# Performance work log

Measured on AMD Instinct MI355X. Metric: run time of the kernel, lower is better.

Reference implementation:

```python
import jax, jax.numpy as jnp
import numpy as np

B, C_IN, H, T = 64, 256, 512, 1024
TMAX = 1024
EPS = 1e-5  # torch LayerNorm default


def setup_inputs() -> dict:
    key = jax.random.key(0)
    ks = jax.random.split(key, 8)
    std = 1.0 / np.sqrt(H)
    u = lambda k, shape: jax.random.uniform(k, shape, jnp.float32, -std, std)
    xs = jax.random.normal(ks[0], (B, C_IN, T), jnp.float32)
    # Linear weights (torch layout [out, in]); LayerNorm gamma=0.1, beta=0,
    # except h2h beta[H:2H] = log(Uniform(1, Tmax-1))  (chrono-style init).
    def ln_h2h_bias(k):
        b = jnp.zeros((3 * H,), jnp.float32)
        z = jnp.log(jax.random.uniform(k, (H,), jnp.float32, 1.0, TMAX - 1.0))
        return b.at[H:2 * H].set(z)
    gamma = jnp.full((3 * H,), 0.1, jnp.float32)
    beta0 = jnp.zeros((3 * H,), jnp.float32)
    return {
        "xs": xs,
        "Wx0": u(ks[1], (3 * H, C_IN)), "Wh0": u(ks[2], (3 * H, H)),
        "gx0": gamma, "bx0": beta0, "gh0": gamma, "bh0": ln_h2h_bias(ks[3]),
        "Wx1": u(ks[4], (3 * H, H)), "Wh1": u(ks[5], (3 * H, H)),
        "gx1": gamma, "bx1": beta0, "gh1": gamma, "bh1": ln_h2h_bias(ks[6]),
    }


def _ln(z, g, b):
    m = jnp.mean(z, axis=-1, keepdims=True)
    v = jnp.mean((z - m) ** 2, axis=-1, keepdims=True)
    return (z - m) * jax.lax.rsqrt(v + EPS) * g + b


def _cell(x, h, Wx, Wh, gx, bx, gh, bh):
    gate_x = _ln(x @ Wx.T, gx, bx)          # [B, 3H]
    gate_h = _ln(h @ Wh.T, gh, bh)          # [B, 3H]
    i_r, i_i, i_n = jnp.split(gate_x, 3, axis=-1)
    h_r, h_i, h_n = jnp.split(gate_h, 3, axis=-1)
    r = jax.nn.sigmoid(i_r + h_r)
    ig = jax.nn.sigmoid(i_i + h_i)
    n = jnp.tanh(i_n + r * h_n)
    return n + ig * (h - n)


def reference(xs, Wx0, Wh0, gx0, bx0, gh0, bh0, Wx1, Wh1, gx1, bx1, gh1, bh1):
    p0 = (Wx0, Wh0, gx0, bx0, gh0, bh0)
    p1 = (Wx1, Wh1, gx1, bx1, gh1, bh1)
    xs_t = jnp.transpose(xs, (2, 0, 1))  # [T, B, C_IN]
    h_init = (jnp.zeros((B, H), xs.dtype), jnp.zeros((B, H), xs.dtype))

    def step(carry, x):
        h0, h1 = carry
        h0 = _cell(x, h0, *p0)
        h1 = _cell(h0, h1, *p1)
        return (h0, h1), h1

    _, ys = jax.lax.scan(step, h_init, xs_t)  # [T, B, H]
    return jnp.transpose(ys, (1, 2, 0))       # [B, H, T]
```

## Files before the change

kernel.cpp:

```cpp
#include <hip/hip_runtime.h>
#include <hip/hip_bf16.h>
#include <cstdint>
#include <cstddef>


#define NBATCH 64
#define HDIM   512
#define THREE_H 1536
#define CINDIM 256
#define T_STEPS 1024
#define EPSLN 1e-5f
#define NBLK 64

typedef __bf16 bf8v __attribute__((ext_vector_type(8)));
typedef float f4 __attribute__((ext_vector_type(4)));
typedef float f2 __attribute__((ext_vector_type(2)));
typedef unsigned int u32x4 __attribute__((ext_vector_type(4)));

static constexpr size_t OFF_BAR    = 0;
static constexpr size_t OFF_ST0P   = 8192;
static constexpr size_t OFF_ST1P   = 24576;
static constexpr size_t OFF_ST2P   = 40960;
static constexpr size_t OFF_H0BF   = 57344;
static constexpr size_t OFF_H1BF   = 122880;
static constexpr size_t OFF_STATSX = 188416;
static constexpr size_t OFF_WH0HI  = 712704;
static constexpr size_t OFF_WH0LO  = OFF_WH0HI + 1572864;
static constexpr size_t OFF_WX1HI  = OFF_WH0LO + 1572864;
static constexpr size_t OFF_WX1LO  = OFF_WX1HI + 1572864;
static constexpr size_t OFF_WH1HI  = OFF_WX1LO + 1572864;
static constexpr size_t OFF_WH1LO  = OFF_WH1HI + 1572864;
static constexpr size_t OFF_WX0HI  = OFF_WH1LO + 1572864;
static constexpr size_t OFF_WX0LO  = OFF_WX0HI + 786432;
static constexpr size_t OFF_XST    = OFF_WX0LO + 786432;
static constexpr size_t OFF_GX0    = OFF_XST + 33554432;

__device__ __forceinline__ f4 mf(bf8v a, bf8v b, f4 c){
  return __builtin_amdgcn_mfma_f32_16x16x32_bf16(a, b, c, 0, 0, 0);
}
__device__ __forceinline__ float sigf(float x){ return 1.0f/(1.0f + __expf(-x)); }
__device__ __forceinline__ float tanhfast(float x){ return 1.0f - 2.0f/(__expf(2.0f*x) + 1.0f); }

__device__ __forceinline__ bf8v ld16_cross(const void* p){
  u32x4 t;
  asm volatile("global_load_dwordx4 %0, %1, off sc0 sc1" : "=v"(t) : "v"(p));
  return __builtin_bit_cast(bf8v, t);
}
__device__ __forceinline__ f4 ld16f_cross(const float* p){
  f4 v;
  asm volatile("global_load_dwordx4 %0, %1, off sc0 sc1" : "=v"(v) : "v"(p));
  return v;
}
__device__ __forceinline__ void st2_cross(__hip_bfloat16* p, unsigned int u){
  asm volatile("global_store_short %0, %1, off sc0 sc1" :: "v"(p), "v"(u));
}
__device__ __forceinline__ void st8f_cross(float* p, f2 v){
  asm volatile("global_store_dwordx2 %0, %1, off sc0 sc1" :: "v"(p), "v"(v));
}
__device__ __forceinline__ void vm_drain(){
  asm volatile("s_waitcnt vmcnt(0)" ::: "memory");
  __builtin_amdgcn_sched_barrier(0);
}

__device__ __forceinline__ void gbar(unsigned int* flags, unsigned int target){
  asm volatile("s_waitcnt vmcnt(0) lgkmcnt(0)" ::: "memory");
  __syncthreads();
  if (threadIdx.x == 0){
    unsigned int* myf = flags + (size_t)blockIdx.x * 32;
    asm volatile("global_store_dword %0, %1, off sc0 sc1" :: "v"(myf), "v"(target) : "memory");
  }
  const int lane = threadIdx.x & 63;
  const unsigned int* pf = flags + (size_t)lane * 32;
  for (;;){
    unsigned int v;
    asm volatile("global_load_dword %0, %1, off sc0 sc1\n\ts_waitcnt vmcnt(0)"
                 : "=v"(v) : "v"(pf) : "memory");
    if (__all((int)(v >= target))) break;
    __builtin_amdgcn_s_sleep(1);
  }
}

__global__ void k_zero(unsigned int* p, int nwords){
  for (int i = blockIdx.x*blockDim.x + threadIdx.x; i < nwords; i += gridDim.x*blockDim.x)
    p[i] = 0u;
}

__global__ void k_conv(const float* __restrict__ src, __hip_bfloat16* __restrict__ hi,
                       __hip_bfloat16* __restrict__ lo, int n){
  for (int i = blockIdx.x*blockDim.x + threadIdx.x; i < n; i += gridDim.x*blockDim.x){
    float w = src[i];
    __hip_bfloat16 h = __float2bfloat16(w);
    hi[i] = h;
    lo[i] = __float2bfloat16(w - __bfloat162float(h));
  }
}

__global__ void k_tr(const float* __restrict__ xs, __hip_bfloat16* __restrict__ xsT){
  const int total = NBATCH * CINDIM * (T_STEPS/4);
  for (int idx = blockIdx.x*blockDim.x + threadIdx.x; idx < total; idx += gridDim.x*blockDim.x){
    int b  = idx >> 16;
    int c  = (idx >> 8) & 255;
    int t4 = idx & 255;
    const float4 v = *(const float4*)(xs + ((size_t)b*CINDIM + c)*T_STEPS + t4*4);
    float vv[4] = {v.x, v.y, v.z, v.w};
    #pragma unroll
    for (int i = 0; i < 4; ++i)
      xsT[(size_t)(4*t4 + i)*(NBATCH*CINDIM) + b*CINDIM + c] = __float2bfloat16(vv[i]);
  }
}

__global__ __launch_bounds__(256,1) void k_xgemm(unsigned char* __restrict__ ws){
  const int tid = threadIdx.x;
  const int bx = blockIdx.x;
  const int t = bx >> 4, s = bx & 15;
  const int lane = tid & 63, w = tid >> 6, l15 = lane & 15, lg = lane >> 4;

  const __hip_bfloat16* X  = (const __hip_bfloat16*)(ws + OFF_XST) + (size_t)t*(NBATCH*CINDIM);
  const __hip_bfloat16* WH = (const __hip_bfloat16*)(ws + OFF_WX0HI);
  const __hip_bfloat16* WL = (const __hip_bfloat16*)(ws + OFF_WX0LO);
  float* statsX = (float*)(ws + OFF_STATSX);
  __hip_bfloat16* GX0 = (__hip_bfloat16*)(ws + OFF_GX0) + (size_t)t*(NBATCH*THREE_H);

  __shared__ __hip_bfloat16 SB[2][2][96][72];

  f4 acc[6];
  #pragma unroll
  for (int i = 0; i < 6; ++i) acc[i] = f4{0.f,0.f,0.f,0.f};

  bf8v A0[8];
  #pragma unroll
  for (int kk = 0; kk < 8; ++kk)
    A0[kk] = *(const bf8v*)(X + (16*w + l15)*CINDIM + kk*32 + 8*lg);

  bf8v pre[6];
  #pragma unroll
  for (int rep = 0; rep < 6; ++rep){
    int idx = tid + rep*256; int half = idx >= 768 ? 1 : 0; int i2 = idx - half*768;
    int rr = i2 >> 3, ko = (i2 & 7)*8;
    int j = 32*s + (rr & 31) + 512*(rr >> 5);
    const __hip_bfloat16* sp = (half ? WL : WH) + (size_t)j*CINDIM;
    pre[rep] = *(const bf8v*)(sp + ko);
  }
  #pragma unroll
  for (int chk = 0; chk < 4; ++chk){
    #pragma unroll
    for (int rep = 0; rep < 6; ++rep){
      int idx = tid + rep*256; int half = idx >= 768 ? 1 : 0; int i2 = idx - half*768;
      int rr = i2 >> 3, ko = (i2 & 7)*8;
      *(bf8v*)&SB[chk & 1][half][rr][ko] = pre[rep];
    }
    __syncthreads();
    if (chk < 3){
      #pragma unroll
      for (int rep = 0; rep < 6; ++rep){
        int idx = tid + rep*256; int half = idx >= 768 ? 1 : 0; int i2 = idx - half*768;
        int rr = i2 >> 3, ko = (i2 & 7)*8;
        int j = 32*s + (rr & 31) + 512*(rr >> 5);
        const __hip_bfloat16* sp = (half ? WL : WH) + (size_t)j*CINDIM;
        pre[rep] = *(const bf8v*)(sp + (chk+1)*64 + ko);
      }
    }
    #pragma unroll
    for (int sub = 0; sub < 2; ++sub){
      int kk = 2*chk + sub; int ko = 32*sub + 8*lg;
      bf8v a = A0[kk];
      #pragma unroll
      for (int nf = 0; nf < 6; ++nf){
        bf8v bh = *(const bf8v*)&SB[chk & 1][0][16*nf + l15][ko];
        bf8v bl = *(const bf8v*)&SB[chk & 1][1][16*nf + l15][ko];
        acc[nf] = mf(a, bh, acc[nf]);
        acc[nf] = mf(a, bl, acc[nf]);
      }
    }
  }

  #pragma unroll
  for (int r = 0; r < 4; ++r){
    int row = 16*w + 4*lg + r;
    float sm = 0.f, sq = 0.f;
    #pragma unroll
    for (int nf = 0; nf < 6; ++nf){
      float v = acc[nf][r];
      sm += v; sq += v*v;
      int tc = 16*nf + l15;
      int j = 32*s + (tc & 31) + 512*(tc >> 5);
      GX0[(size_t)row*THREE_H + j] = __float2bfloat16(v);
    }
    #pragma unroll
    for (int m = 1; m < 16; m <<= 1){ sm += __shfl_xor(sm, m); sq += __shfl_xor(sq, m); }
    if (l15 == 0){
      atomicAdd(&statsX[((size_t)t*64 + row)*2 + 0], sm);
      atomicAdd(&statsX[((size_t)t*64 + row)*2 + 1], sq);
    }
  }
}

__global__ void k_statsx(float* __restrict__ sx){
  int i = blockIdx.x*blockDim.x + threadIdx.x;
  if (i < T_STEPS*NBATCH){
    float s = sx[2*i], q = sx[2*i+1];
    float m = s * (1.0f/1536.0f);
    float v = fmaxf(q * (1.0f/1536.0f) - m*m, 0.0f);
    sx[2*i] = m;
    sx[2*i+1] = rsqrtf(v + EPSLN);
  }
}


__device__ __forceinline__ void runA(
    int s, unsigned char* ws, f4* red, f2* BC0,
    const float* gxg, const float* gxb, const float* ghg, const float* ghb)
{
  const int tid = threadIdx.x, lane = tid & 63, w = tid >> 6;
  const int l15 = lane & 15, lg = (lane >> 4) & 3;

  unsigned int* flags = (unsigned int*)(ws + OFF_BAR);
  float* st0P = (float*)(ws + OFF_ST0P);
  __hip_bfloat16* h0bf = (__hip_bfloat16*)(ws + OFF_H0BF);
  const float* statsX = (const float*)(ws + OFF_STATSX);
  const __hip_bfloat16* GX0 = (const __hip_bfloat16*)(ws + OFF_GX0);

  bf8v BW[3][4][2];
  {
    const __hip_bfloat16* hi = (const __hip_bfloat16*)(ws + OFF_WH0HI);
    const __hip_bfloat16* lo = (const __hip_bfloat16*)(ws + OFF_WH0LO);
    #pragma unroll
    for (int g = 0; g < 3; ++g){
      const size_t j = (size_t)(16*s + l15 + 512*g);
      #pragma unroll
      for (int kt = 0; kt < 4; ++kt){
        const size_t ko = (size_t)((4*w + kt)*32 + 8*lg);
        BW[g][kt][0] = *(const bf8v*)(hi + j*HDIM + ko);
        BW[g][kt][1] = *(const bf8v*)(lo + j*HDIM + ko);
      }
    }
  }
  float PXg[3], PXb[3], PHg[3], PHb[3];
  #pragma unroll
  for (int g = 0; g < 3; ++g){
    int j = 16*s + l15 + 512*g;
    PXg[g] = gxg[j]; PXb[g] = gxb[j]; PHg[g] = ghg[j]; PHb[g] = ghb[j];
  }

  float hp[4] = {0.f,0.f,0.f,0.f};
  unsigned int bc = 0;

  for (int tau = 0; tau <= T_STEPS; ++tau){
    const bool act = (tau < T_STEPS);
    f4 zx[3];
    float gxraw[3][4], mxv[4], rsxv[4];

    if (act){
      bf8v AR[4][4];
      #pragma unroll
      for (int rt = 0; rt < 4; ++rt)
        #pragma unroll
        for (int kt = 0; kt < 4; ++kt)
          AR[rt][kt] = ld16_cross(h0bf + (size_t)(16*rt + l15)*HDIM + (4*w + kt)*32 + 8*lg);
      vm_drain();

      f4 AC[3][4];
      #pragma unroll
      for (int g = 0; g < 3; ++g)
        #pragma unroll
        for (int rt = 0; rt < 4; ++rt) AC[g][rt] = f4{0.f,0.f,0.f,0.f};
      #pragma unroll
      for (int kt = 0; kt < 4; ++kt)
        #pragma unroll
        for (int g = 0; g < 3; ++g)
          #pragma unroll
          for (int rt = 0; rt < 4; ++rt){
            AC[g][rt] = mf(AR[rt][kt], BW[g][kt][0], AC[g][rt]);
            AC[g][rt] = mf(AR[rt][kt], BW[g][kt][1], AC[g][rt]);
          }

      #pragma unroll
      for (int r = 0; r < 4; ++r){
        int row = 16*w + 4*lg + r;
        mxv[r]  = statsX[((size_t)tau*64 + row)*2 + 0];
        rsxv[r] = statsX[((size_t)tau*64 + row)*2 + 1];
        #pragma unroll
        for (int g = 0; g < 3; ++g)
          gxraw[g][r] = __bfloat162float(
            GX0[(size_t)tau*(NBATCH*THREE_H) + (size_t)row*THREE_H + (16*s + l15 + 512*g)]);
      }

      #pragma unroll
      for (int g = 0; g < 3; ++g)
        #pragma unroll
        for (int rt = 0; rt < 4; ++rt)
          red[((w*3 + g)*4 + rt)*64 + lane] = AC[g][rt];
      __syncthreads();
      #pragma unroll
      for (int g = 0; g < 3; ++g){
        f4 a = red[((0*3 + g)*4 + w)*64 + lane];
        a += red[((1*3 + g)*4 + w)*64 + lane];
        a += red[((2*3 + g)*4 + w)*64 + lane];
        a += red[((3*3 + g)*4 + w)*64 + lane];
        zx[g] = a;
      }

      #pragma unroll
      for (int r = 0; r < 4; ++r){
        float s1 = zx[0][r] + zx[1][r] + zx[2][r];
        float q1 = zx[0][r]*zx[0][r] + zx[1][r]*zx[1][r] + zx[2][r]*zx[2][r];
        #pragma unroll
        for (int m = 1; m < 16; m <<= 1){ s1 += __shfl_xor(s1, m); q1 += __shfl_xor(q1, m); }
        if (l15 == 0){
          int row = 16*w + 4*lg + r;
          st8f_cross(st0P + ((size_t)row*32 + s)*2, f2{s1, q1});
        }
      }
    }

    gbar(flags, ++bc);

    if (act){
      {
        int row = tid >> 2, q = tid & 3;
        const float* bp = st0P + (size_t)row*64 + q*16;
        f4 v0 = ld16f_cross(bp),   v1 = ld16f_cross(bp+4);
        f4 v2 = ld16f_cross(bp+8), v3 = ld16f_cross(bp+12);
        vm_drain();
        float sm = v0[0]+v0[2]+v1[0]+v1[2]+v2[0]+v2[2]+v3[0]+v3[2];
        float sq = v0[1]+v0[3]+v1[1]+v1[3]+v2[1]+v2[3]+v3[1]+v3[3];
        sm += __shfl_xor(sm,1); sq += __shfl_xor(sq,1);
        sm += __shfl_xor(sm,2); sq += __shfl_xor(sq,2);
        if (q == 0){
          float m = sm*(1.0f/1536.0f);
          float vv = fmaxf(sq*(1.0f/1536.0f) - m*m, 0.0f);
          BC0[row] = f2{m, rsqrtf(vv + EPSLN)};
        }
      }
      __syncthreads();
      #pragma unroll
      for (int r = 0; r < 4; ++r){
        int row = 16*w + 4*lg + r;
        f2 mr = BC0[row];
        float m = mr[0], rs = mr[1];
        float ghr = (zx[0][r]-m)*rs*PHg[0] + PHb[0];
        float ghi = (zx[1][r]-m)*rs*PHg[1] + PHb[1];
        float ghn = (zx[2][r]-m)*rs*PHg[2] + PHb[2];
        float gxr = (gxraw[0][r] - mxv[r])*rsxv[r]*PXg[0] + PXb[0];
        float gxi = (gxraw[1][r] - mxv[r])*rsxv[r]*PXg[1] + PXb[1];
        float gxn = (gxraw[2][r] - mxv[r])*rsxv[r]*PXg[2] + PXb[2];
        float rg = sigf(gxr + ghr);
        float ig = sigf(gxi + ghi);
        float nn = tanhfast(gxn + rg*ghn);
        float hn = nn + ig*(hp[r] - nn);
        hp[r] = hn;
        __hip_bfloat16 hb = __float2bfloat16(hn);
        st2_cross(h0bf + (size_t)row*HDIM + 16*s + l15,
                  (unsigned int)*reinterpret_cast<unsigned short*>(&hb));
      }
    }

    gbar(flags, ++bc);
  }
}

__device__ __forceinline__ void runB(
    int s, unsigned char* ws, f4* red, f2* BC1, f2* BC2,
    const float* gxg, const float* gxb, const float* ghg, const float* ghb,
    float* out)
{
  const int tid = threadIdx.x, lane = tid & 63, w = tid >> 6;
  const int l15 = lane & 15, lg = (lane >> 4) & 3;

  unsigned int* flags = (unsigned int*)(ws + OFF_BAR);
  float* st1P = (float*)(ws + OFF_ST1P);
  float* st2P = (float*)(ws + OFF_ST2P);
  __hip_bfloat16* h0bf = (__hip_bfloat16*)(ws + OFF_H0BF);
  __hip_bfloat16* h1bf = (__hip_bfloat16*)(ws + OFF_H1BF);

  bf8v BW[6][4][2];
  {
    const __hip_bfloat16* hix = (const __hip_bfloat16*)(ws + OFF_WX1HI);
    const __hip_bfloat16* lox = (const __hip_bfloat16*)(ws + OFF_WX1LO);
    const __hip_bfloat16* hih = (const __hip_bfloat16*)(ws + OFF_WH1HI);
    const __hip_bfloat16* loh = (const __hip_bfloat16*)(ws + OFF_WH1LO);
    #pragma unroll
    for (int g = 0; g < 3; ++g){
      const size_t j = (size_t)(16*s + l15 + 512*g);
      #pragma unroll
      for (int kt = 0; kt < 4; ++kt){
        const size_t ko = (size_t)((4*w + kt)*32 + 8*lg);
        BW[g][kt][0]   = *(const bf8v*)(hix + j*HDIM + ko);
        BW[g][kt][1]   = *(const bf8v*)(lox + j*HDIM + ko);
        BW[3+g][kt][0] = *(const bf8v*)(hih + j*HDIM + ko);
        BW[3+g][kt][1] = *(const bf8v*)(loh + j*HDIM + ko);
      }
    }
  }
  float PXg[3], PXb[3], PHg[3], PHb[3];
  #pragma unroll
  for (int g = 0; g < 3; ++g){
    int j = 16*s + l15 + 512*g;
    PXg[g] = gxg[j]; PXb[g] = gxb[j]; PHg[g] = ghg[j]; PHb[g] = ghb[j];
  }

  float hp[4] = {0.f,0.f,0.f,0.f};
  unsigned int bc = 0;

  for (int tau = 0; tau <= T_STEPS; ++tau){
    const bool act = (tau >= 1);
    f4 zx[3], zh[3];

    if (act){
      bf8v AR[4][4];
      #pragma unroll
      for (int rt = 0; rt < 4; ++rt)
        #pragma unroll
        for (int kt = 0; kt < 4; ++kt)
          AR[rt][kt] = ld16_cross(h0bf + (size_t)(16*rt + l15)*HDIM + (4*w + kt)*32 + 8*lg);
      vm_drain();

      f4 AC[3][4];
      #pragma unroll
      for (int g = 0; g < 3; ++g)
        #pragma unroll
        for (int rt = 0; rt < 4; ++rt) AC[g][rt] = f4{0.f,0.f,0.f,0.f};
      #pragma unroll
      for (int kt = 0; kt < 4; ++kt)
        #pragma unroll
        for (int g = 0; g < 3; ++g)
          #pragma unroll
          for (int rt = 0; rt < 4; ++rt){
            AC[g][rt] = mf(AR[rt][kt], BW[g][kt][0], AC[g][rt]);
            AC[g][rt] = mf(AR[rt][kt], BW[g][kt][1], AC[g][rt]);
          }
      #pragma unroll
      for (int g = 0; g < 3; ++g)
        #pragma unroll
        for (int rt = 0; rt < 4; ++rt)
          red[((w*3 + g)*4 + rt)*64 + lane] = AC[g][rt];

      #pragma unroll
      for (int rt = 0; rt < 4; ++rt)
        #pragma unroll
        for (int kt = 0; kt < 4; ++kt)
          AR[rt][kt] = ld16_cross(h1bf + (size_t)(16*rt + l15)*HDIM + (4*w + kt)*32 + 8*lg);

      __syncthreads();
      #pragma unroll
      for (int g = 0; g < 3; ++g){
        f4 a = red[((0*3 + g)*4 + w)*64 + lane];
        a += red[((1*3 + g)*4 + w)*64 + lane];
        a += red[((2*3 + g)*4 + w)*64 + lane];
        a += red[((3*3 + g)*4 + w)*64 + lane];
        zx[g] = a;
      }
      __syncthreads();

      vm_drain();
      #pragma unroll
      for (int g = 0; g < 3; ++g)
        #pragma unroll
        for (int rt = 0; rt < 4; ++rt) AC[g][rt] = f4{0.f,0.f,0.f,0.f};
      #pragma unroll
      for (int kt = 0; kt < 4; ++kt)
        #pragma unroll
        for (int g = 0; g < 3; ++g)
          #pragma unroll
          for (int rt = 0; rt < 4; ++rt){
            AC[g][rt] = mf(AR[rt][kt], BW[3+g][kt][0], AC[g][rt]);
            AC[g][rt] = mf(AR[rt][kt], BW[3+g][kt][1], AC[g][rt]);
          }
      #pragma unroll
      for (int g = 0; g < 3; ++g)
        #pragma unroll
        for (int rt = 0; rt < 4; ++rt)
          red[((w*3 + g)*4 + rt)*64 + lane] = AC[g][rt];
      __syncthreads();
      #pragma unroll
      for (int g = 0; g < 3; ++g){
        f4 a = red[((0*3 + g)*4 + w)*64 + lane];
        a += red[((1*3 + g)*4 + w)*64 + lane];
        a += red[((2*3 + g)*4 + w)*64 + lane];
        a += red[((3*3 + g)*4 + w)*64 + lane];
        zh[g] = a;
      }

      #pragma unroll
      for (int r = 0; r < 4; ++r){
        float s1 = zx[0][r] + zx[1][r] + zx[2][r];
        float q1 = zx[0][r]*zx[0][r] + zx[1][r]*zx[1][r] + zx[2][r]*zx[2][r];
        float s2 = zh[0][r] + zh[1][r] + zh[2][r];
        float q2 = zh[0][r]*zh[0][r] + zh[1][r]*zh[1][r] + zh[2][r]*zh[2][r];
        #pragma unroll
        for (int m = 1; m < 16; m <<= 1){
          s1 += __shfl_xor(s1, m); q1 += __shfl_xor(q1, m);
          s2 += __shfl_xor(s2, m); q2 += __shfl_xor(q2, m);
        }
        if (l15 == 0){
          int row = 16*w + 4*lg + r;
          st8f_cross(st1P + ((size_t)row*32 + s)*2, f2{s1, q1});
          st8f_cross(st2P + ((size_t)row*32 + s)*2, f2{s2, q2});
        }
      }
    }

    gbar(flags, ++bc);

    if (act){
      const int t1 = tau - 1;
      {
        int row = tid >> 2, q = tid & 3;
        const float* b1 = st1P + (size_t)row*64 + q*16;
        const float* b2 = st2P + (size_t)row*64 + q*16;
        f4 a0 = ld16f_cross(b1),   a1 = ld16f_cross(b1+4);
        f4 a2 = ld16f_cross(b1+8), a3 = ld16f_cross(b1+12);
        f4 c0 = ld16f_cross(b2),   c1 = ld16f_cross(b2+4);
        f4 c2 = ld16f_cross(b2+8), c3 = ld16f_cross(b2+12);
        vm_drain();
        float s1 = a0[0]+a0[2]+a1[0]+a1[2]+a2[0]+a2[2]+a3[0]+a3[2];
        float q1 = a0[1]+a0[3]+a1[1]+a1[3]+a2[1]+a2[3]+a3[1]+a3[3];
        float s2 = c0[0]+c0[2]+c1[0]+c1[2]+c2[0]+c2[2]+c3[0]+c3[2];
        float q2 = c0[1]+c0[3]+c1[1]+c1[3]+c2[1]+c2[3]+c3[1]+c3[3];
        s1 += __shfl_xor(s1,1); q1 += __shfl_xor(q1,1);
        s1 += __shfl_xor(s1,2); q1 += __shfl_xor(q1,2);
        s2 += __shfl_xor(s2,1); q2 += __shfl_xor(q2,1);
        s2 += __shfl_xor(s2,2); q2 += __shfl_xor(q2,2);
        if (q == 0){
          float m1 = s1*(1.0f/1536.0f);
          float v1 = fmaxf(q1*(1.0f/1536.0f) - m1*m1, 0.0f);
          BC1[row] = f2{m1, rsqrtf(v1 + EPSLN)};
          float m2 = s2*(1.0f/1536.0f);
          float v2 = fmaxf(q2*(1.0f/1536.0f) - m2*m2, 0.0f);
          BC2[row] = f2{m2, rsqrtf(v2 + EPSLN)};
        }
      }
      __syncthreads();
      #pragma unroll
      for (int r = 0; r < 4; ++r){
        int row = 16*w + 4*lg + r;
        f2 m1 = BC1[row], m2 = BC2[row];
        float gxr = (zx[0][r] - m1[0])*m1[1]*PXg[0] + PXb[0];
        float gxi = (zx[1][r] - m1[0])*m1[1]*PXg[1] + PXb[1];
        float gxn = (zx[2][r] - m1[0])*m1[1]*PXg[2] + PXb[2];
        float ghr = (zh[0][r] - m2[0])*m2[1]*PHg[0] + PHb[0];
        float ghi = (zh[1][r] - m2[0])*m2[1]*PHg[1] + PHb[1];
        float ghn = (zh[2][r] - m2[0])*m2[1]*PHg[2] + PHb[2];
        float rg = sigf(gxr + ghr);
        float ig = sigf(gxi + ghi);
        float nn = tanhfast(gxn + rg*ghn);
        float hn = nn + ig*(hp[r] - nn);
        hp[r] = hn;
        int j = 16*s + l15;
        __hip_bfloat16 hb = __float2bfloat16(hn);
        st2_cross(h1bf + (size_t)row*HDIM + j,
                  (unsigned int)*reinterpret_cast<unsigned short*>(&hb));
        out[(size_t)row*(HDIM*T_STEPS) + (size_t)j*T_STEPS + t1] = hn;
      }
    }

    gbar(flags, ++bc);
  }
}

__global__ __launch_bounds__(256,1) void k_rnn(
    const float* __restrict__ gx0g, const float* __restrict__ gx0b,
    const float* __restrict__ gh0g, const float* __restrict__ gh0b,
    const float* __restrict__ gx1g, const float* __restrict__ gx1b,
    const float* __restrict__ gh1g, const float* __restrict__ gh1b,
    unsigned char* __restrict__ ws, float* __restrict__ out)
{
  __shared__ f4 red[4*3*4*64];
  __shared__ f2 BCa[64];
  __shared__ f2 BCb[64];

  const int bi = blockIdx.x;
  if (bi < 32)
    runA(bi, ws, red, BCa, gx0g, gx0b, gh0g, gh0b);
  else
    runB(bi - 32, ws, red, BCa, BCb, gx1g, gx1b, gh1g, gh1b, out);
}

extern "C" void kernel_launch(void* const* d_in, const int* in_sizes, int n_in,
                              void* d_out, int out_size, void* d_ws, size_t ws_size,
                              hipStream_t stream) {
  const float* xs  = (const float*)d_in[0];
  const float* Wx0 = (const float*)d_in[1];
  const float* Wh0 = (const float*)d_in[2];
  const float* gx0g = (const float*)d_in[3];
  const float* gx0b = (const float*)d_in[4];
  const float* gh0g = (const float*)d_in[5];
  const float* gh0b = (const float*)d_in[6];
  const float* Wx1 = (const float*)d_in[7];
  const float* Wh1 = (const float*)d_in[8];
  const float* gx1g = (const float*)d_in[9];
  const float* gx1b = (const float*)d_in[10];
  const float* gh1g = (const float*)d_in[11];
  const float* gh1b = (const float*)d_in[12];

  unsigned char* ws = (unsigned char*)d_ws;
  float* out = (float*)d_out;
  (void)in_sizes; (void)n_in; (void)out_size; (void)ws_size;

  k_zero<<<256, 256, 0, stream>>>((unsigned int*)ws, (int)(OFF_WH0HI/4));

  k_conv<<<512, 256, 0, stream>>>(Wh0, (__hip_bfloat16*)(ws+OFF_WH0HI), (__hip_bfloat16*)(ws+OFF_WH0LO), THREE_H*HDIM);
  k_conv<<<512, 256, 0, stream>>>(Wx1, (__hip_bfloat16*)(ws+OFF_WX1HI), (__hip_bfloat16*)(ws+OFF_WX1LO), THREE_H*HDIM);
  k_conv<<<512, 256, 0, stream>>>(Wh1, (__hip_bfloat16*)(ws+OFF_WH1HI), (__hip_bfloat16*)(ws+OFF_WH1LO), THREE_H*HDIM);
  k_conv<<<512, 256, 0, stream>>>(Wx0, (__hip_bfloat16*)(ws+OFF_WX0HI), (__hip_bfloat16*)(ws+OFF_WX0LO), THREE_H*CINDIM);

  k_tr<<<4096, 256, 0, stream>>>(xs, (__hip_bfloat16*)(ws+OFF_XST));

  k_xgemm<<<16384, 256, 0, stream>>>(ws);
  k_statsx<<<256, 256, 0, stream>>>((float*)(ws+OFF_STATSX));

  k_rnn<<<NBLK, 256, 0, stream>>>(gx0g, gx0b, gh0g, gh0b, gx1g, gx1b, gh1g, gh1b, ws, out);
}
```

Before: 13.02 ms.

## Replace global barriers with per-group flags, epoch-tagged stats, and multi-buffered hidden states

Removes the two full-grid barriers per timestep and replaces them with point-to-point flag polling. Layer-0 blocks wait only on their own group and on layer 1 being at most three steps behind. Layer-1 blocks wait on the matching layer-0 step. LayerNorm partial stats now carry an epoch tag, so readers spin on the data itself instead of a barrier. h0 is ring-buffered four deep and h1 double-buffered, letting the two layers run decoupled and pipelined, at the cost of more workspace and spin-polling traffic.

```diff
diff --git a/kernel.cpp b/kernel.cpp
--- a/kernel.cpp
+++ b/kernel.cpp
@@ -11,6 +11,7 @@
 #define T_STEPS 1024
 #define EPSLN 1e-5f
 #define NBLK 64
+#define HSZ (NBATCH*HDIM)
 
 typedef __bf16 bf8v __attribute__((ext_vector_type(8)));
 typedef float f4 __attribute__((ext_vector_type(4)));
@@ -18,13 +19,13 @@
 typedef unsigned int u32x4 __attribute__((ext_vector_type(4)));
 
 static constexpr size_t OFF_BAR    = 0;
-static constexpr size_t OFF_ST0P   = 8192;
-static constexpr size_t OFF_ST1P   = 24576;
-static constexpr size_t OFF_ST2P   = 40960;
-static constexpr size_t OFF_H0BF   = 57344;
-static constexpr size_t OFF_H1BF   = 122880;
-static constexpr size_t OFF_STATSX = 188416;
-static constexpr size_t OFF_WH0HI  = 712704;
+static constexpr size_t OFF_STA    = 8192;
+static constexpr size_t OFF_STB1   = 40960;
+static constexpr size_t OFF_STB2   = 73728;
+static constexpr size_t OFF_H0BF   = 106496;
+static constexpr size_t OFF_H1BF   = 368640;
+static constexpr size_t OFF_STATSX = 499712;
+static constexpr size_t OFF_WH0HI  = 1024000;
 static constexpr size_t OFF_WH0LO  = OFF_WH0HI + 1572864;
 static constexpr size_t OFF_WX1HI  = OFF_WH0LO + 1572864;
 static constexpr size_t OFF_WX1LO  = OFF_WX1HI + 1572864;
@@ -54,30 +55,30 @@
 __device__ __forceinline__ void st2_cross(__hip_bfloat16* p, unsigned int u){
   asm volatile("global_store_short %0, %1, off sc0 sc1" :: "v"(p), "v"(u));
 }
-__device__ __forceinline__ void st8f_cross(float* p, f2 v){
-  asm volatile("global_store_dwordx2 %0, %1, off sc0 sc1" :: "v"(p), "v"(v));
+__device__ __forceinline__ void st16f_cross(float* p, f4 v){
+  asm volatile("global_store_dwordx4 %0, %1, off sc0 sc1" :: "v"(p), "v"(v));
 }
 __device__ __forceinline__ void vm_drain(){
   asm volatile("s_waitcnt vmcnt(0)" ::: "memory");
   __builtin_amdgcn_sched_barrier(0);
 }
 
-__device__ __forceinline__ void gbar(unsigned int* flags, unsigned int target){
-  asm volatile("s_waitcnt vmcnt(0) lgkmcnt(0)" ::: "memory");
-  __syncthreads();
-  if (threadIdx.x == 0){
-    unsigned int* myf = flags + (size_t)blockIdx.x * 32;
-    asm volatile("global_store_dword %0, %1, off sc0 sc1" :: "v"(myf), "v"(target) : "memory");
-  }
+__device__ __forceinline__ void dualpoll(const unsigned int* flags, unsigned tA, unsigned tB){
   const int lane = threadIdx.x & 63;
   const unsigned int* pf = flags + (size_t)lane * 32;
+  const unsigned tgt = (lane < 32) ? tA : tB;
   for (;;){
     unsigned int v;
     asm volatile("global_load_dword %0, %1, off sc0 sc1\n\ts_waitcnt vmcnt(0)"
                  : "=v"(v) : "v"(pf) : "memory");
-    if (__all((int)(v >= target))) break;
+    if (__all((int)(v >= tgt))) break;
     __builtin_amdgcn_s_sleep(1);
   }
+}
+
+__device__ __forceinline__ void pubflag(unsigned int* flags, int line, unsigned val){
+  unsigned int* p = flags + (size_t)line * 32;
+  asm volatile("global_store_dword %0, %1, off sc0 sc1" :: "v"(p), "v"(val) : "memory");
 }
 
 __global__ void k_zero(unsigned int* p, int nwords){
@@ -215,7 +216,7 @@
   const int l15 = lane & 15, lg = (lane >> 4) & 3;
 
   unsigned int* flags = (unsigned int*)(ws + OFF_BAR);
-  float* st0P = (float*)(ws + OFF_ST0P);
+  float* stA = (float*)(ws + OFF_STA);
   __hip_bfloat16* h0bf = (__hip_bfloat16*)(ws + OFF_H0BF);
   const float* statsX = (const float*)(ws + OFF_STATSX);
   const __hip_bfloat16* GX0 = (const __hip_bfloat16*)(ws + OFF_GX0);
@@ -243,119 +244,130 @@
   }
 
   float hp[4] = {0.f,0.f,0.f,0.f};
-  unsigned int bc = 0;
-
-  for (int tau = 0; tau <= T_STEPS; ++tau){
-    const bool act = (tau < T_STEPS);
-    f4 zx[3];
-    float gxraw[3][4], mxv[4], rsxv[4];
-
-    if (act){
-      bf8v AR[4][4];
-      #pragma unroll
-      for (int rt = 0; rt < 4; ++rt)
-        #pragma unroll
-        for (int kt = 0; kt < 4; ++kt)
-          AR[rt][kt] = ld16_cross(h0bf + (size_t)(16*rt + l15)*HDIM + (4*w + kt)*32 + 8*lg);
-      vm_drain();
-
-      f4 AC[3][4];
+
+  for (int t = 0; t < T_STEPS; ++t){
+    const float ef = (float)(t + 1);
+    const unsigned tB = (t >= 3) ? (unsigned)(t - 3) : 0u;
+
+    dualpoll(flags, (unsigned)t, tB);
+
+    const __hip_bfloat16* h0r = h0bf + (size_t)((t + 3) & 3) * HSZ;
+    __hip_bfloat16*       h0w = h0bf + (size_t)(t & 3) * HSZ;
+
+    bf8v AR[4][4];
+    #pragma unroll
+    for (int rt = 0; rt < 4; ++rt)
+      #pragma unroll
+      for (int kt = 0; kt < 4; ++kt)
+        AR[rt][kt] = ld16_cross(h0r + (size_t)(16*rt + l15)*HDIM + (4*w + kt)*32 + 8*lg);
+    vm_drain();
+
+    f4 AC[3][4];
+    #pragma unroll
+    for (int g = 0; g < 3; ++g)
+      #pragma unroll
+      for (int rt = 0; rt < 4; ++rt) AC[g][rt] = f4{0.f,0.f,0.f,0.f};
+    #pragma unroll
+    for (int kt = 0; kt < 4; ++kt)
       #pragma unroll
       for (int g = 0; g < 3; ++g)
         #pragma unroll
-        for (int rt = 0; rt < 4; ++rt) AC[g][rt] = f4{0.f,0.f,0.f,0.f};
-      #pragma unroll
-      for (int kt = 0; kt < 4; ++kt)
+        for (int rt = 0; rt < 4; ++rt){
+          AC[g][rt] = mf(AR[rt][kt], BW[g][kt][0], AC[g][rt]);
+          AC[g][rt] = mf(AR[rt][kt], BW[g][kt][1], AC[g][rt]);
+        }
+
+    float gxraw[3][4], mxv[4], rsxv[4];
+    #pragma unroll
+    for (int r = 0; r < 4; ++r){
+      int row = 16*w + 4*lg + r;
+      mxv[r]  = statsX[((size_t)t*64 + row)*2 + 0];
+      rsxv[r] = statsX[((size_t)t*64 + row)*2 + 1];
+      #pragma unroll
+      for (int g = 0; g < 3; ++g)
+        gxraw[g][r] = __bfloat162float(
+          GX0[(size_t)t*(NBATCH*THREE_H) + (size_t)row*THREE_H + (16*s + l15 + 512*g)]);
+    }
+
+    f4 zx[3];
+    #pragma unroll
+    for (int g = 0; g < 3; ++g)
+      #pragma unroll
+      for (int rt = 0; rt < 4; ++rt)
+        red[((w*3 + g)*4 + rt)*64 + lane] = AC[g][rt];
+    __syncthreads();
+    #pragma unroll
+    for (int g = 0; g < 3; ++g){
+      f4 a = red[((0*3 + g)*4 + w)*64 + lane];
+      a += red[((1*3 + g)*4 + w)*64 + lane];
+      a += red[((2*3 + g)*4 + w)*64 + lane];
+      a += red[((3*3 + g)*4 + w)*64 + lane];
+      zx[g] = a;
+    }
+
+    #pragma unroll
+    for (int r = 0; r < 4; ++r){
+      float s1 = zx[0][r] + zx[1][r] + zx[2][r];
+      float q1 = zx[0][r]*zx[0][r] + zx[1][r]*zx[1][r] + zx[2][r]*zx[2][r];
+      #pragma unroll
+      for (int m = 1; m < 16; m <<= 1){ s1 += __shfl_xor(s1, m); q1 += __shfl_xor(q1, m); }
+      if (l15 == 0){
+        int row = 16*w + 4*lg + r;
+        st16f_cross(stA + ((size_t)row*32 + s)*4, f4{s1, q1, ef, 0.f});
+      }
+    }
+
+    {
+      int row = tid >> 2, q = tid & 3;
+      const float* bp = stA + ((size_t)row*32 + q*8)*4;
+      f4 v[8];
+      for (;;){
         #pragma unroll
-        for (int g = 0; g < 3; ++g)
-          #pragma unroll
-          for (int rt = 0; rt < 4; ++rt){
-            AC[g][rt] = mf(AR[rt][kt], BW[g][kt][0], AC[g][rt]);
-            AC[g][rt] = mf(AR[rt][kt], BW[g][kt][1], AC[g][rt]);
-          }
-
-      #pragma unroll
-      for (int r = 0; r < 4; ++r){
-        int row = 16*w + 4*lg + r;
-        mxv[r]  = statsX[((size_t)tau*64 + row)*2 + 0];
-        rsxv[r] = statsX[((size_t)tau*64 + row)*2 + 1];
+        for (int i = 0; i < 8; ++i) v[i] = ld16f_cross(bp + i*4);
+        vm_drain();
+        bool ok = true;
         #pragma unroll
-        for (int g = 0; g < 3; ++g)
-          gxraw[g][r] = __bfloat162float(
-            GX0[(size_t)tau*(NBATCH*THREE_H) + (size_t)row*THREE_H + (16*s + l15 + 512*g)]);
-      }
-
-      #pragma unroll
-      for (int g = 0; g < 3; ++g)
-        #pragma unroll
-        for (int rt = 0; rt < 4; ++rt)
-          red[((w*3 + g)*4 + rt)*64 + lane] = AC[g][rt];
-      __syncthreads();
-      #pragma unroll
-      for (int g = 0; g < 3; ++g){
-        f4 a = red[((0*3 + g)*4 + w)*64 + lane];
-        a += red[((1*3 + g)*4 + w)*64 + lane];
-        a += red[((2*3 + g)*4 + w)*64 + lane];
-        a += red[((3*3 + g)*4 + w)*64 + lane];
-        zx[g] = a;
-      }
-
-      #pragma unroll
-      for (int r = 0; r < 4; ++r){
-        float s1 = zx[0][r] + zx[1][r] + zx[2][r];
-        float q1 = zx[0][r]*zx[0][r] + zx[1][r]*zx[1][r] + zx[2][r]*zx[2][r];
-        #pragma unroll
-        for (int m = 1; m < 16; m <<= 1){ s1 += __shfl_xor(s1, m); q1 += __shfl_xor(q1, m); }
-        if (l15 == 0){
-          int row = 16*w + 4*lg + r;
-          st8f_cross(st0P + ((size_t)row*32 + s)*2, f2{s1, q1});
-        }
-      }
-    }
-
-    gbar(flags, ++bc);
-
-    if (act){
-      {
-        int row = tid >> 2, q = tid & 3;
-        const float* bp = st0P + (size_t)row*64 + q*16;
-        f4 v0 = ld16f_cross(bp),   v1 = ld16f_cross(bp+4);
-        f4 v2 = ld16f_cross(bp+8), v3 = ld16f_cross(bp+12);
-        vm_drain();
-        float sm = v0[0]+v0[2]+v1[0]+v1[2]+v2[0]+v2[2]+v3[0]+v3[2];
-        float sq = v0[1]+v0[3]+v1[1]+v1[3]+v2[1]+v2[3]+v3[1]+v3[3];
-        sm += __shfl_xor(sm,1); sq += __shfl_xor(sq,1);
-        sm += __shfl_xor(sm,2); sq += __shfl_xor(sq,2);
-        if (q == 0){
-          float m = sm*(1.0f/1536.0f);
-          float vv = fmaxf(sq*(1.0f/1536.0f) - m*m, 0.0f);
-          BC0[row] = f2{m, rsqrtf(vv + EPSLN)};
-        }
-      }
-      __syncthreads();
-      #pragma unroll
-      for (int r = 0; r < 4; ++r){
-        int row = 16*w + 4*lg + r;
-        f2 mr = BC0[row];
-        float m = mr[0], rs = mr[1];
-        float ghr = (zx[0][r]-m)*rs*PHg[0] + PHb[0];
-        float ghi = (zx[1][r]-m)*rs*PHg[1] + PHb[1];
-        float ghn = (zx[2][r]-m)*rs*PHg[2] + PHb[2];
-        float gxr = (gxraw[0][r] - mxv[r])*rsxv[r]*PXg[0] + PXb[0];
-        float gxi = (gxraw[1][r] - mxv[r])*rsxv[r]*PXg[1] + PXb[1];
-        float gxn = (gxraw[2][r] - mxv[r])*rsxv[r]*PXg[2] + PXb[2];
-        float rg = sigf(gxr + ghr);
-        float ig = sigf(gxi + ghi);
-        float nn = tanhfast(gxn + rg*ghn);
-        float hn = nn + ig*(hp[r] - nn);
-        hp[r] = hn;
-        __hip_bfloat16 hb = __float2bfloat16(hn);
-        st2_cross(h0bf + (size_t)row*HDIM + 16*s + l15,
-                  (unsigned int)*reinterpret_cast<unsigned short*>(&hb));
-      }
-    }
-
-    gbar(flags, ++bc);
+        for (int i = 0; i < 8; ++i) ok = ok && (v[i][2] >= ef);
+        if (__all((int)ok)) break;
+        __builtin_amdgcn_s_sleep(1);
+      }
+      float sm = 0.f, sq = 0.f;
+      #pragma unroll
+      for (int i = 0; i < 8; ++i){ sm += v[i][0]; sq += v[i][1]; }
+      sm += __shfl_xor(sm,1); sq += __shfl_xor(sq,1);
+      sm += __shfl_xor(sm,2); sq += __shfl_xor(sq,2);
+      if (q == 0){
+        float m = sm*(1.0f/1536.0f);
+        float vv = fmaxf(sq*(1.0f/1536.0f) - m*m, 0.0f);
+        BC0[row] = f2{m, rsqrtf(vv + EPSLN)};
+      }
+    }
+    __syncthreads();
+
+    #pragma unroll
+    for (int r = 0; r < 4; ++r){
+      int row = 16*w + 4*lg + r;
+      f2 mr = BC0[row];
+      float m = mr[0], rs = mr[1];
+      float ghr = (zx[0][r]-m)*rs*PHg[0] + PHb[0];
+      float ghi = (zx[1][r]-m)*rs*PHg[1] + PHb[1];
+      float ghn = (zx[2][r]-m)*rs*PHg[2] + PHb[2];
+      float gxr = (gxraw[0][r] - mxv[r])*rsxv[r]*PXg[0] + PXb[0];
+      float gxi = (gxraw[1][r] - mxv[r])*rsxv[r]*PXg[1] + PXb[1];
+      float gxn = (gxraw[2][r] - mxv[r])*rsxv[r]*PXg[2] + PXb[2];
+      float rg = sigf(gxr + ghr);
+      float ig = sigf(gxi + ghi);
+      float nn = tanhfast(gxn + rg*ghn);
+      float hn = nn + ig*(hp[r] - nn);
+      hp[r] = hn;
+      __hip_bfloat16 hb = __float2bfloat16(hn);
+      st2_cross(h0w + (size_t)row*HDIM + 16*s + l15,
+                (unsigned int)*reinterpret_cast<unsigned short*>(&hb));
+    }
+
+    vm_drain();
+    __syncthreads();
+    if (tid == 0) pubflag(flags, s, (unsigned)(t + 1));
   }
 }
 
@@ -368,8 +380,8 @@
   const int l15 = lane & 15, lg = (lane >> 4) & 3;
 
   unsigned int* flags = (unsigned int*)(ws + OFF_BAR);
-  float* st1P = (float*)(ws + OFF_ST1P);
-  float* st2P = (float*)(ws + OFF_ST2P);
+  float* stB1 = (float*)(ws + OFF_STB1);
+  float* stB2 = (float*)(ws + OFF_STB2);
   __hip_bfloat16* h0bf = (__hip_bfloat16*)(ws + OFF_H0BF);
   __hip_bfloat16* h1bf = (__hip_bfloat16*)(ws + OFF_H1BF);
 
@@ -400,161 +412,172 @@
   }
 
   float hp[4] = {0.f,0.f,0.f,0.f};
-  unsigned int bc = 0;
-
-  for (int tau = 0; tau <= T_STEPS; ++tau){
-    const bool act = (tau >= 1);
+
+  for (int tau = 1; tau <= T_STEPS; ++tau){
+    const float ef = (float)tau;
+
+    dualpoll(flags, (unsigned)tau, (unsigned)(tau - 1));
+
+    const __hip_bfloat16* h0r = h0bf + (size_t)((tau + 3) & 3) * HSZ;
+    const __hip_bfloat16* h1r = h1bf + (size_t)(tau & 1) * HSZ;
+    __hip_bfloat16*       h1w = h1bf + (size_t)((tau + 1) & 1) * HSZ;
+
     f4 zx[3], zh[3];
 
-    if (act){
-      bf8v AR[4][4];
-      #pragma unroll
-      for (int rt = 0; rt < 4; ++rt)
-        #pragma unroll
-        for (int kt = 0; kt < 4; ++kt)
-          AR[rt][kt] = ld16_cross(h0bf + (size_t)(16*rt + l15)*HDIM + (4*w + kt)*32 + 8*lg);
-      vm_drain();
-
-      f4 AC[3][4];
+    bf8v AR[4][4];
+    #pragma unroll
+    for (int rt = 0; rt < 4; ++rt)
+      #pragma unroll
+      for (int kt = 0; kt < 4; ++kt)
+        AR[rt][kt] = ld16_cross(h0r + (size_t)(16*rt + l15)*HDIM + (4*w + kt)*32 + 8*lg);
+    vm_drain();
+
+    f4 AC[3][4];
+    #pragma unroll
+    for (int g = 0; g < 3; ++g)
+      #pragma unroll
+      for (int rt = 0; rt < 4; ++rt) AC[g][rt] = f4{0.f,0.f,0.f,0.f};
+    #pragma unroll
+    for (int kt = 0; kt < 4; ++kt)
       #pragma unroll
       for (int g = 0; g < 3; ++g)
         #pragma unroll
-        for (int rt = 0; rt < 4; ++rt) AC[g][rt] = f4{0.f,0.f,0.f,0.f};
+        for (int rt = 0; rt < 4; ++rt){
+          AC[g][rt] = mf(AR[rt][kt], BW[g][kt][0], AC[g][rt]);
+          AC[g][rt] = mf(AR[rt][kt], BW[g][kt][1], AC[g][rt]);
+        }
+    #pragma unroll
+    for (int g = 0; g < 3; ++g)
+      #pragma unroll
+      for (int rt = 0; rt < 4; ++rt)
+        red[((w*3 + g)*4 + rt)*64 + lane] = AC[g][rt];
+
+    #pragma unroll
+    for (int rt = 0; rt < 4; ++rt)
       #pragma unroll
       for (int kt = 0; kt < 4; ++kt)
-        #pragma unroll
-        for (int g = 0; g < 3; ++g)
-          #pragma unroll
-          for (int rt = 0; rt < 4; ++rt){
-            AC[g][rt] = mf(AR[rt][kt], BW[g][kt][0], AC[g][rt]);
-            AC[g][rt] = mf(AR[rt][kt], BW[g][kt][1], AC[g][rt]);
-          }
+        AR[rt][kt] = ld16_cross(h1r + (size_t)(16*rt + l15)*HDIM + (4*w + kt)*32 + 8*lg);
+
+    __syncthreads();
+    #pragma unroll
+    for (int g = 0; g < 3; ++g){
+      f4 a = red[((0*3 + g)*4 + w)*64 + lane];
+      a += red[((1*3 + g)*4 + w)*64 + lane];
+      a += red[((2*3 + g)*4 + w)*64 + lane];
+      a += red[((3*3 + g)*4 + w)*64 + lane];
+      zx[g] = a;
+    }
+    __syncthreads();
+
+    vm_drain();
+    #pragma unroll
+    for (int g = 0; g < 3; ++g)
+      #pragma unroll
+      for (int rt = 0; rt < 4; ++rt) AC[g][rt] = f4{0.f,0.f,0.f,0.f};
+    #pragma unroll
+    for (int kt = 0; kt < 4; ++kt)
       #pragma unroll
       for (int g = 0; g < 3; ++g)
         #pragma unroll
-        for (int rt = 0; rt < 4; ++rt)
-          red[((w*3 + g)*4 + rt)*64 + lane] = AC[g][rt];
-
+        for (int rt = 0; rt < 4; ++rt){
+          AC[g][rt] = mf(AR[rt][kt], BW[3+g][kt][0], AC[g][rt]);
+          AC[g][rt] = mf(AR[rt][kt], BW[3+g][kt][1], AC[g][rt]);
+        }
+    #pragma unroll
+    for (int g = 0; g < 3; ++g)
       #pragma unroll
       for (int rt = 0; rt < 4; ++rt)
+        red[((w*3 + g)*4 + rt)*64 + lane] = AC[g][rt];
+    __syncthreads();
+    #pragma unroll
+    for (int g = 0; g < 3; ++g){
+      f4 a = red[((0*3 + g)*4 + w)*64 + lane];
+      a += red[((1*3 + g)*4 + w)*64 + lane];
+      a += red[((2*3 + g)*4 + w)*64 + lane];
+      a += red[((3*3 + g)*4 + w)*64 + lane];
+      zh[g] = a;
+    }
+
+    #pragma unroll
+    for (int r = 0; r < 4; ++r){
+      float s1 = zx[0][r] + zx[1][r] + zx[2][r];
+      float q1 = zx[0][r]*zx[0][r] + zx[1][r]*zx[1][r] + zx[2][r]*zx[2][r];
+      float s2 = zh[0][r] + zh[1][r] + zh[2][r];
+      float q2 = zh[0][r]*zh[0][r] + zh[1][r]*zh[1][r] + zh[2][r]*zh[2][r];
+      #pragma unroll
+      for (int m = 1; m < 16; m <<= 1){
+        s1 += __shfl_xor(s1, m); q1 += __shfl_xor(q1, m);
+        s2 += __shfl_xor(s2, m); q2 += __shfl_xor(q2, m);
+      }
+      if (l15 == 0){
+        int row = 16*w + 4*lg + r;
+        st16f_cross(stB1 + ((size_t)row*32 + s)*4, f4{s1, q1, ef, 0.f});
+        st16f_cross(stB2 + ((size_t)row*32 + s)*4, f4{s2, q2, ef, 0.f});
+      }
+    }
+
+    {
+      int row = tid >> 2, q = tid & 3;
+      const float* b1 = stB1 + ((size_t)row*32 + q*8)*4;
+      const float* b2 = stB2 + ((size_t)row*32 + q*8)*4;
+      f4 v1[8], v2[8];
+      for (;;){
         #pragma unroll
-        for (int kt = 0; kt < 4; ++kt)
-          AR[rt][kt] = ld16_cross(h1bf + (size_t)(16*rt + l15)*HDIM + (4*w + kt)*32 + 8*lg);
-
-      __syncthreads();
-      #pragma unroll
-      for (int g = 0; g < 3; ++g){
-        f4 a = red[((0*3 + g)*4 + w)*64 + lane];
-        a += red[((1*3 + g)*4 + w)*64 + lane];
-        a += red[((2*3 + g)*4 + w)*64 + lane];
-        a += red[((3*3 + g)*4 + w)*64 + lane];
-        zx[g] = a;
-      }
-      __syncthreads();
-
-      vm_drain();
-      #pragma unroll
-      for (int g = 0; g < 3; ++g)
+        for (int i = 0; i < 8; ++i){ v1[i] = ld16f_cross(b1 + i*4); v2[i] = ld16f_cross(b2 + i*4); }
+        vm_drain();
+        bool ok = true;
         #pragma unroll
-        for (int rt = 0; rt < 4; ++rt) AC[g][rt] = f4{0.f,0.f,0.f,0.f};
-      #pragma unroll
-      for (int kt = 0; kt < 4; ++kt)
-        #pragma unroll
-        for (int g = 0; g < 3; ++g)
-          #pragma unroll
-          for (int rt = 0; rt < 4; ++rt){
-            AC[g][rt] = mf(AR[rt][kt], BW[3+g][kt][0], AC[g][rt]);
-            AC[g][rt] = mf(AR[rt][kt], BW[3+g][kt][1], AC[g][rt]);
-          }
-      #pragma unroll
-      for (int g = 0; g < 3; ++g)
-        #pragma unroll
-        for (int rt = 0; rt < 4; ++rt)
-          red[((w*3 + g)*4 + rt)*64 + lane] = AC[g][rt];
-      __syncthreads();
-      #pragma unroll
-      for (int g = 0; g < 3; ++g){
-        f4 a = red[((0*3 + g)*4 + w)*64 + lane];
-        a += red[((1*3 + g)*4 + w)*64 + lane];
-        a += red[((2*3 + g)*4 + w)*64 + lane];
-        a += red[((3*3 + g)*4 + w)*64 + lane];
-        zh[g] = a;
-      }
-
-      #pragma unroll
-      for (int r = 0; r < 4; ++r){
-        float s1 = zx[0][r] + zx[1][r] + zx[2][r];
-        float q1 = zx[0][r]*zx[0][r] + zx[1][r]*zx[1][r] + zx[2][r]*zx[2][r];
-        float s2 = zh[0][r] + zh[1][r] + zh[2][r];
-        float q2 = zh[0][r]*zh[0][r] + zh[1][r]*zh[1][r] + zh[2][r]*zh[2][r];
-        #pragma unroll
-        for (int m = 1; m < 16; m <<= 1){
-          s1 += __shfl_xor(s1, m); q1 += __shfl_xor(q1, m);
-          s2 += __shfl_xor(s2, m); q2 += __shfl_xor(q2, m);
-        }
-        if (l15 == 0){
-          int row = 16*w + 4*lg + r;
-          st8f_cross(st1P + ((size_t)row*32 + s)*2, f2{s1, q1});
-          st8f_cross(st2P + ((size_t)row*32 + s)*2, f2{s2, q2});
-        }
-      }
-    }
-
-    gbar(flags, ++bc);
-
-    if (act){
-      const int t1 = tau - 1;
-      {
-        int row = tid >> 2, q = tid & 3;
-        const float* b1 = st1P + (size_t)row*64 + q*16;
-        const float* b2 = st2P + (size_t)row*64 + q*16;
-        f4 a0 = ld16f_cross(b1),   a1 = ld16f_cross(b1+4);
-        f4 a2 = ld16f_cross(b1+8), a3 = ld16f_cross(b1+12);
-        f4 c0 = ld16f_cross(b2),   c1 = ld16f_cross(b2+4);
-        f4 c2 = ld16f_cross(b2+8), c3 = ld16f_cross(b2+12);
-        vm_drain();
-        float s1 = a0[0]+a0[2]+a1[0]+a1[2]+a2[0]+a2[2]+a3[0]+a3[2];
-        float q1 = a0[1]+a0[3]+a1[1]+a1[3]+a2[1]+a2[3]+a3[1]+a3[3];
-        float s2 = c0[0]+c0[2]+c1[0]+c1[2]+c2[0]+c2[2]+c3[0]+c3[2];
-        float q2 = c0[1]+c0[3]+c1[1]+c1[3]+c2[1]+c2[3]+c3[1]+c3[3];
-        s1 += __shfl_xor(s1,1); q1 += __shfl_xor(q1,1);
-        s1 += __shfl_xor(s1,2); q1 += __shfl_xor(q1,2);
-        s2 += __shfl_xor(s2,1); q2 += __shfl_xor(q2,1);
-        s2 += __shfl_xor(s2,2); q2 += __shfl_xor(q2,2);
-        if (q == 0){
-          float m1 = s1*(1.0f/1536.0f);
-          float v1 = fmaxf(q1*(1.0f/1536.0f) - m1*m1, 0.0f);
-          BC1[row] = f2{m1, rsqrtf(v1 + EPSLN)};
-          float m2 = s2*(1.0f/1536.0f);
-          float v2 = fmaxf(q2*(1.0f/1536.0f) - m2*m2, 0.0f);
-          BC2[row] = f2{m2, rsqrtf(v2 + EPSLN)};
-        }
-      }
-      __syncthreads();
-      #pragma unroll
-      for (int r = 0; r < 4; ++r){
-        int row = 16*w + 4*lg + r;
-        f2 m1 = BC1[row], m2 = BC2[row];
-        float gxr = (zx[0][r] - m1[0])*m1[1]*PXg[0] + PXb[0];
-        float gxi = (zx[1][r] - m1[0])*m1[1]*PXg[1] + PXb[1];
-        float gxn = (zx[2][r] - m1[0])*m1[1]*PXg[2] + PXb[2];
-        float ghr = (zh[0][r] - m2[0])*m2[1]*PHg[0] + PHb[0];
-        float ghi = (zh[1][r] - m2[0])*m2[1]*PHg[1] + PHb[1];
-        float ghn = (zh[2][r] - m2[0])*m2[1]*PHg[2] + PHb[2];
-        float rg = sigf(gxr + ghr);
-        float ig = sigf(gxi + ghi);
-        float nn = tanhfast(gxn + rg*ghn);
-        float hn = nn + ig*(hp[r] - nn);
-        hp[r] = hn;
-        int j = 16*s + l15;
-        __hip_bfloat16 hb = __float2bfloat16(hn);
-        st2_cross(h1bf + (size_t)row*HDIM + j,
-                  (unsigned int)*reinterpret_cast<unsigned short*>(&hb));
-        out[(size_t)row*(HDIM*T_STEPS) + (size_t)j*T_STEPS + t1] = hn;
-      }
-    }
-
-    gbar(flags, ++bc);
+        for (int i = 0; i < 8; ++i) ok = ok && (v1[i][2] >= ef) && (v2[i][2] >= ef);
+        if (__all((int)ok)) break;
+        __builtin_amdgcn_s_sleep(1);
+      }
+      float s1 = 0.f, q1 = 0.f, s2 = 0.f, q2 = 0.f;
+      #pragma unroll
+      for (int i = 0; i < 8; ++i){
+        s1 += v1[i][0]; q1 += v1[i][1];
+        s2 += v2[i][0]; q2 += v2[i][1];
+      }
+      s1 += __shfl_xor(s1,1); q1 += __shfl_xor(q1,1);
+      s1 += __shfl_xor(s1,2); q1 += __shfl_xor(q1,2);
+      s2 += __shfl_xor(s2,1); q2 += __shfl_xor(q2,1);
+      s2 += __shfl_xor(s2,2); q2 += __shfl_xor(q2,2);
+      if (q == 0){
+        float m1 = s1*(1.0f/1536.0f);
+        float vv1 = fmaxf(q1*(1.0f/1536.0f) - m1*m1, 0.0f);
+        BC1[row] = f2{m1, rsqrtf(vv1 + EPSLN)};
+        float m2 = s2*(1.0f/1536.0f);
+        float vv2 = fmaxf(q2*(1.0f/1536.0f) - m2*m2, 0.0f);
+        BC2[row] = f2{m2, rsqrtf(vv2 + EPSLN)};
+      }
+    }
+    __syncthreads();
+
+    const int t1 = tau - 1;
+    #pragma unroll
+    for (int r = 0; r < 4; ++r){
+      int row = 16*w + 4*lg + r;
+      f2 m1 = BC1[row], m2 = BC2[row];
+      float gxr = (zx[0][r] - m1[0])*m1[1]*PXg[0] + PXb[0];
+      float gxi = (zx[1][r] - m1[0])*m1[1]*PXg[1] + PXb[1];
+      float gxn = (zx[2][r] - m1[0])*m1[1]*PXg[2] + PXb[2];
+      float ghr = (zh[0][r] - m2[0])*m2[1]*PHg[0] + PHb[0];
+      float ghi = (zh[1][r] - m2[0])*m2[1]*PHg[1] + PHb[1];
+      float ghn = (zh[2][r] - m2[0])*m2[1]*PHg[2] + PHb[2];
+      float rg = sigf(gxr + ghr);
+      float ig = sigf(gxi + ghi);
+      float nn = tanhfast(gxn + rg*ghn);
+      float hn = nn + ig*(hp[r] - nn);
+      hp[r] = hn;
+      int j = 16*s + l15;
+      __hip_bfloat16 hb = __float2bfloat16(hn);
+      st2_cross(h1w + (size_t)row*HDIM + j,
+                (unsigned int)*reinterpret_cast<unsigned short*>(&hb));
+      out[(size_t)row*(HDIM*T_STEPS) + (size_t)j*T_STEPS + t1] = hn;
+    }
+
+    vm_drain();
+    __syncthreads();
+    if (tid == 0) pubflag(flags, 32 + s, (unsigned)tau);
   }
 }
 
```

Result: slower. 16.62 ms (+27.6%).
